# Kernel optimization log

Hardware: AMD Instinct MI355X
Metric: run time of the kernel (lower is better)

## Reference

```python
import jax, jax.numpy as jnp
import numpy as np

B = 8192
NUM_NODES = 100000
EMB = 128
W1D, W2D, W3D = 64, 128, 256   # witness_dims
CODE = 128
HID = 64                        # hardcoded hidden_dim in WitnessExtractor / decoder
TOTW = W1D + W2D + W3D          # 448


def _linear_params(key, fan_in, fan_out):
    k1, k2 = jax.random.split(key)
    bound = 1.0 / np.sqrt(fan_in)
    w = jax.random.uniform(k1, (fan_out, fan_in), jnp.float32, -bound, bound)
    b = jax.random.uniform(k2, (fan_out,), jnp.float32, -bound, bound)
    return w, b


def setup_inputs() -> dict:
    key = jax.random.key(0)
    ks = jax.random.split(key, 12)
    u = jax.random.randint(ks[0], (B,), 0, NUM_NODES, dtype=jnp.int64 if jax.config.jax_enable_x64 else jnp.int32)
    v = jax.random.randint(ks[1], (B,), 0, NUM_NODES, dtype=u.dtype)
    emb = jax.random.normal(ks[2], (NUM_NODES, EMB), jnp.float32)
    e1_w1, e1_b1 = _linear_params(ks[3], 2 * EMB, HID)
    e1_w2, e1_b2 = _linear_params(ks[4], HID, W1D)
    e2_w1, e2_b1 = _linear_params(ks[5], 2 * EMB + W1D, HID)
    e2_w2, e2_b2 = _linear_params(ks[6], HID, W2D)
    e3_w1, e3_b1 = _linear_params(ks[7], 2 * EMB + W2D, HID)
    e3_w2, e3_b2 = _linear_params(ks[8], HID, W3D)
    trop_w = jax.random.normal(ks[9], (CODE, TOTW), jnp.float32)  # init_scale=1.0
    dec_w1, dec_b1 = _linear_params(ks[10], CODE, HID)
    dec_w2, dec_b2 = _linear_params(ks[11], HID, 1)
    return dict(u=u, v=v, emb=emb,
                e1_w1=e1_w1, e1_b1=e1_b1, e1_w2=e1_w2, e1_b2=e1_b2,
                e2_w1=e2_w1, e2_b1=e2_b1, e2_w2=e2_w2, e2_b2=e2_b2,
                e3_w1=e3_w1, e3_b1=e3_b1, e3_w2=e3_w2, e3_b2=e3_b2,
                trop_w=trop_w, dec_w1=dec_w1, dec_b1=dec_b1,
                dec_w2=dec_w2, dec_b2=dec_b2)


def _witness(x, w1, b1, w2, b2):
    h = jax.nn.relu(x @ w1.T + b1)
    return jax.nn.sigmoid(h @ w2.T + b2)


def reference(u, v, emb,
              e1_w1, e1_b1, e1_w2, e1_b2,
              e2_w1, e2_b1, e2_w2, e2_b2,
              e3_w1, e3_b1, e3_w2, e3_b2,
              trop_w, dec_w1, dec_b1, dec_w2, dec_b2):
    u_emb = emb[u]                               # [B, EMB]
    v_emb = emb[v]
    base = jnp.concatenate([u_emb, v_emb], axis=1)  # [B, 2*EMB]
    w1 = _witness(base, e1_w1, e1_b1, e1_w2, e1_b2)
    w2 = _witness(jnp.concatenate([base, w1], axis=1), e2_w1, e2_b1, e2_w2, e2_b2)
    w3 = _witness(jnp.concatenate([base, w2], axis=1), e3_w1, e3_b1, e3_w2, e3_b2)
    wit = jnp.concatenate([w1, w2, w3], axis=1)  # [B, TOTW]
    # tropical (min-plus) matmul: code[b,o] = min_j (wit[b,j] + trop_w[o,j])
    code = jnp.min(wit[:, None, :] + trop_w[None, :, :], axis=2)  # [B, CODE]
    h = jax.nn.relu(code @ dec_w1.T + dec_b1)
    return h @ dec_w2.T + dec_b2                 # [B, 1]
```

## Files before the change

### kernel.cpp

```cpp
#include <hip/hip_runtime.h>
#include <hip/hip_fp16.h>
#include <math.h>

#define BATCH 8192
#define EMB 128
#define TILE 16
#define NTHREADS 1024
#define NWAVES 16
#define CH 136
#define WITS 450
#define SLOT 32

#define OFF_E1W1 0
#define OFF_E1W2 16384
#define OFF_E2W1 20480
#define OFF_E2W2 40960
#define OFF_E3W1 49152
#define OFF_E3W2 73728
#define OFF_DW1  90112
#define OFF_DW2  98304
#define W_DENSE  98368

typedef __attribute__((ext_vector_type(8))) _Float16 v8h;
typedef __attribute__((ext_vector_type(4))) float v4f;

struct Smem {
    _Float16 XB[32 * CH];
    _Float16 W12C[24 * CH];
    _Float16 H[8 * CH];
    _Float16 CODE[16 * CH];
    _Float16 WITrm[TILE * WITS];
    unsigned int ent[128 * SLOT];
    unsigned int cnt[128];
};

__global__ __launch_bounds__(1024) void prep_kernel(
    const float* __restrict__ s0, const float* __restrict__ s1,
    const float* __restrict__ s2, const float* __restrict__ s3,
    const float* __restrict__ s4, const float* __restrict__ s5,
    const float* __restrict__ s6, const float* __restrict__ s7,
    const float* __restrict__ trop, _Float16* __restrict__ ws)
{
    const int b = blockIdx.x;
    const int tid = threadIdx.x;
    if (b < 25) {
        const int idx4 = (b * 1024 + tid) * 4;
        if (idx4 >= W_DENSE) return;
        const float* src; int off;
        if      (idx4 < OFF_E1W2) { src = s0; off = OFF_E1W1; }
        else if (idx4 < OFF_E2W1) { src = s1; off = OFF_E1W2; }
        else if (idx4 < OFF_E2W2) { src = s2; off = OFF_E2W1; }
        else if (idx4 < OFF_E3W1) { src = s3; off = OFF_E2W2; }
        else if (idx4 < OFF_E3W2) { src = s4; off = OFF_E3W1; }
        else if (idx4 < OFF_DW1)  { src = s5; off = OFF_E3W2; }
        else if (idx4 < OFF_DW2)  { src = s6; off = OFF_DW1;  }
        else                      { src = s7; off = OFF_DW2;  }
        const float4 v = *(const float4*)(src + (idx4 - off));
        _Float16* dst = ws + idx4;
        dst[0] = (_Float16)v.x; dst[1] = (_Float16)v.y;
        dst[2] = (_Float16)v.z; dst[3] = (_Float16)v.w;
    } else {
        const int lane = tid & 63;
        const int wave = tid >> 6;
        const int o = (b - 25) * 16 + wave;
        if (o >= 128) return;
        unsigned int* base = (unsigned int*)(ws + W_DENSE);

        const float* row = trop + (size_t)o * 448;
        float vals[7];
        float mn = 1e30f;
        #pragma unroll
        for (int it = 0; it < 7; ++it) {
            vals[it] = row[lane + it * 64];
            mn = fminf(mn, vals[it]);
        }
        mn = fminf(mn, __shfl_xor(mn, 1, 64));
        mn = fminf(mn, __shfl_xor(mn, 2, 64));
        mn = fminf(mn, __shfl_xor(mn, 4, 64));
        mn = fminf(mn, __shfl_xor(mn, 8, 64));
        mn = fminf(mn, __shfl_xor(mn, 16, 64));
        mn = fminf(mn, __shfl_xor(mn, 32, 64));
        const float thr = mn + 1.02f;

        const unsigned long long ltmask = (1ull << lane) - 1ull;
        unsigned int pos0 = 0;
        #pragma unroll
        for (int it = 0; it < 7; ++it) {
            const bool sel = vals[it] <= thr;
            const unsigned long long m = __ballot(sel);
            if (sel) {
                const unsigned int pos = pos0 + (unsigned)__popcll(m & ltmask);
                if (pos < SLOT) {
                    const unsigned short hb =
                        __builtin_bit_cast(unsigned short, (_Float16)vals[it]);
                    base[o * SLOT + pos] = ((unsigned)(lane + it * 64) << 16) | hb;
                }
            }
            pos0 += (unsigned)__popcll(m);
        }
        if (lane == 0) base[4096 + o] = pos0;
    }
}

template <int K, int STEPS0, int O, int ACT, bool CHUNKW, bool RMW>
__device__ __forceinline__ void dense_mfma(
    const _Float16* __restrict__ Wg, const float* __restrict__ bias,
    const _Float16* A0, const _Float16* A1,
    _Float16* OutC, _Float16* OutRM, int rmbase, int wave, int lane)
{
    constexpr int STEPS = K / 32;
    static_assert(STEPS % 2 == 0, "even steps");
    constexpr int NJOBS = O / 16;
    const int l15 = lane & 15;
    const int quad = lane >> 4;

    for (int nt = wave; nt < NJOBS; nt += NWAVES) {
        v4f c0 = {0.f, 0.f, 0.f, 0.f};
        v4f c1 = {0.f, 0.f, 0.f, 0.f};
        const _Float16* wrow = Wg + (size_t)(nt * 16 + l15) * K + quad * 8;
        #pragma unroll
        for (int s = 0; s < STEPS; s += 2) {
            const int g0 = s * 4 + quad;
            const int g1 = (s + 1) * 4 + quad;
            const _Float16* a0p = (s < STEPS0)
                ? (A0 + g0 * CH + l15 * 8)
                : (A1 + (g0 - STEPS0 * 4) * CH + l15 * 8);
            const _Float16* a1p = ((s + 1) < STEPS0)
                ? (A0 + g1 * CH + l15 * 8)
                : (A1 + (g1 - STEPS0 * 4) * CH + l15 * 8);
            const v8h a0 = *(const v8h*)a0p;
            const v8h b0 = *(const v8h*)(wrow + s * 32);
            const v8h a1 = *(const v8h*)a1p;
            const v8h b1 = *(const v8h*)(wrow + (s + 1) * 32);
            c0 = __builtin_amdgcn_mfma_f32_16x16x32_f16(a0, b0, c0, 0, 0, 0);
            c1 = __builtin_amdgcn_mfma_f32_16x16x32_f16(a1, b1, c1, 0, 0, 0);
        }
        const v4f c = c0 + c1;
        const int o = nt * 16 + l15;
        const float bs = bias[o];
        #pragma unroll
        for (int i = 0; i < 4; ++i) {
            float vv = c[i] + bs;
            if (ACT == 0) vv = fmaxf(vv, 0.f);
            else          vv = 1.f / (1.f + __expf(-vv));
            const int m = quad * 4 + i;
            const _Float16 hv = (_Float16)vv;
            if (CHUNKW) OutC[(o >> 3) * CH + m * 8 + (o & 7)] = hv;
            if (RMW)    OutRM[m * WITS + rmbase + o] = hv;
        }
    }
}

__global__ __launch_bounds__(NTHREADS, 8) void tacit_fused_kernel(
    const int* __restrict__ u, const int* __restrict__ v,
    const float* __restrict__ emb,
    const float* __restrict__ e1_b1, const float* __restrict__ e1_b2,
    const float* __restrict__ e2_b1, const float* __restrict__ e2_b2,
    const float* __restrict__ e3_b1, const float* __restrict__ e3_b2,
    const float* __restrict__ dec_b1, const float* __restrict__ dec_b2,
    const float* __restrict__ trop,
    const _Float16* __restrict__ ws,
    float* __restrict__ out)
{
    __shared__ Smem S;
    const int tid = threadIdx.x;
    const int lane = tid & 63;
    const int wave = tid >> 6;
    const int row0 = blockIdx.x * TILE;

    {
        const unsigned int* base = (const unsigned int*)(ws + W_DENSE);
        *(uint4*)&S.ent[tid * 4] = *(const uint4*)(base + tid * 4);
        if (tid < 32) *(uint4*)&S.cnt[tid * 4] = *(const uint4*)(base + 4096 + tid * 4);
    }
    if (tid < 512) {
        const int row = tid & 15;
        const int kq = tid >> 4;
        const int node = (kq < 16) ? u[row0 + row] : v[row0 + row];
        const int col = (kq & 15) * 8;
        const float4 f0 = *(const float4*)(emb + (size_t)node * EMB + col);
        const float4 f1 = *(const float4*)(emb + (size_t)node * EMB + col + 4);
        v8h hv;
        hv[0] = (_Float16)f0.x; hv[1] = (_Float16)f0.y;
        hv[2] = (_Float16)f0.z; hv[3] = (_Float16)f0.w;
        hv[4] = (_Float16)f1.x; hv[5] = (_Float16)f1.y;
        hv[6] = (_Float16)f1.z; hv[7] = (_Float16)f1.w;
        *(v8h*)&S.XB[kq * CH + row * 8] = hv;
    }
    __syncthreads();

    dense_mfma<256, 8, 64, 0, true, false>(ws + OFF_E1W1, e1_b1, S.XB, nullptr,
                                           S.H, nullptr, 0, wave, lane);
    __syncthreads();
    dense_mfma<64, 2, 64, 1, true, true>(ws + OFF_E1W2, e1_b2, S.H, nullptr,
                                         S.W12C, S.WITrm, 0, wave, lane);
    __syncthreads();

    dense_mfma<320, 8, 64, 0, true, false>(ws + OFF_E2W1, e2_b1, S.XB, S.W12C,
                                           S.H, nullptr, 0, wave, lane);
    __syncthreads();
    dense_mfma<64, 2, 128, 1, true, true>(ws + OFF_E2W2, e2_b2, S.H, nullptr,
                                          S.W12C + 8 * CH, S.WITrm, 64, wave, lane);
    __syncthreads();

    dense_mfma<384, 8, 64, 0, true, false>(ws + OFF_E3W1, e3_b1, S.XB, S.W12C + 8 * CH,
                                           S.H, nullptr, 0, wave, lane);
    __syncthreads();
    dense_mfma<64, 2, 256, 1, false, true>(ws + OFF_E3W2, e3_b2, S.H, nullptr,
                                           nullptr, S.WITrm, 192, wave, lane);
    __syncthreads();

    {
        const int r = lane & 15;
        const int cp = lane >> 4;
        const _Float16* wrow = &S.WITrm[r * WITS];
        float acc[8];
        int idx[8], end8[8];
        #pragma unroll
        for (int i = 0; i < 8; ++i) {
            const int o = (wave << 3) + i;
            const int n = (int)S.cnt[o];
            idx[i] = o * SLOT + cp;
            end8[i] = o * SLOT + (n < SLOT ? n : SLOT);
            acc[i] = 1e30f;
        }
        bool any = true;
        while (any) {
            any = false;
            #pragma unroll
            for (int i = 0; i < 8; ++i) {
                if (idx[i] < end8[i]) {
                    const unsigned int cwv = S.ent[idx[i]];
                    const int j = (int)(cwv >> 16);
                    const float tv = (float)__builtin_bit_cast(
                        _Float16, (unsigned short)(cwv & 0xffffu));
                    acc[i] = fminf(acc[i], (float)wrow[j] + tv);
                    idx[i] += 4;
                    any = true;
                }
            }
        }
        #pragma unroll
        for (int i = 0; i < 8; ++i) {
            const int o = (wave << 3) + i;
            if ((int)S.cnt[o] > SLOT) {
                const float* trow = trop + (size_t)o * 448;
                for (int j = cp; j < 448; j += 4)
                    acc[i] = fminf(acc[i], (float)wrow[j] + trow[j]);
            }
        }
        #pragma unroll
        for (int i = 0; i < 8; ++i) {
            float a = acc[i];
            a = fminf(a, __shfl_xor(a, 16, 64));
            a = fminf(a, __shfl_xor(a, 32, 64));
            if (cp == 0) {
                const int o = (wave << 3) + i;
                S.CODE[(o >> 3) * CH + r * 8 + (o & 7)] = (_Float16)a;
            }
        }
    }
    __syncthreads();

    dense_mfma<128, 4, 64, 0, true, false>(ws + OFF_DW1, dec_b1, S.CODE, nullptr,
                                           S.H, nullptr, 0, wave, lane);
    __syncthreads();

    if (tid < 64) {
        const int r = lane & 15;
        const int part = lane >> 4;
        const _Float16* w2 = ws + OFF_DW2;
        float s = 0.f;
        #pragma unroll
        for (int q = 0; q < 2; ++q) {
            const int c = part + q * 4;
            const v8h hr = *(const v8h*)(&S.H[c * CH + r * 8]);
            const v8h wr = *(const v8h*)(w2 + c * 8);
            #pragma unroll
            for (int t = 0; t < 8; ++t) s += (float)hr[t] * (float)wr[t];
        }
        s += __shfl_xor(s, 16, 64);
        s += __shfl_xor(s, 32, 64);
        if (part == 0) out[row0 + r] = s + dec_b2[0];
    }
}

extern "C" void kernel_launch(void* const* d_in, const int* in_sizes, int n_in,
                              void* d_out, int out_size, void* d_ws, size_t ws_size,
                              hipStream_t stream) {
    const int*   u      = (const int*)d_in[0];
    const int*   v      = (const int*)d_in[1];
    const float* emb    = (const float*)d_in[2];
    const float* e1_w1  = (const float*)d_in[3];
    const float* e1_b1  = (const float*)d_in[4];
    const float* e1_w2  = (const float*)d_in[5];
    const float* e1_b2  = (const float*)d_in[6];
    const float* e2_w1  = (const float*)d_in[7];
    const float* e2_b1  = (const float*)d_in[8];
    const float* e2_w2  = (const float*)d_in[9];
    const float* e2_b2  = (const float*)d_in[10];
    const float* e3_w1  = (const float*)d_in[11];
    const float* e3_b1  = (const float*)d_in[12];
    const float* e3_w2  = (const float*)d_in[13];
    const float* e3_b2  = (const float*)d_in[14];
    const float* trop_w = (const float*)d_in[15];
    const float* dec_w1 = (const float*)d_in[16];
    const float* dec_b1 = (const float*)d_in[17];
    const float* dec_w2 = (const float*)d_in[18];
    const float* dec_b2 = (const float*)d_in[19];
    float* out = (float*)d_out;
    _Float16* ws = (_Float16*)d_ws;

    prep_kernel<<<33, 1024, 0, stream>>>(
        e1_w1, e1_w2, e2_w1, e2_w2, e3_w1, e3_w2, dec_w1, dec_w2, trop_w, ws);

    tacit_fused_kernel<<<BATCH / TILE, NTHREADS, 0, stream>>>(
        u, v, emb,
        e1_b1, e1_b2, e2_b1, e2_b2, e3_b1, e3_b2, dec_b1, dec_b2,
        trop_w, ws, out);
}
```

Baseline: 151.2 us.

## Compute base-embedding parts of all three first-layer projections in one stage

The base-input (u,v embedding) part of the first linear layer of each of the three witness extractors is now computed together in a single stage across 12 waves. Partial sums for extractors 2 and 3 are stored as fp32 in new shared buffers. The later stages then only multiply the witness-dependent columns (64 or 128) and add the stored partials. This moves dependent serial work into one wider parallel stage and shortens the critical path, at the cost of extra LDS, which may reduce occupancy.

```diff
diff --git a/kernel.cpp b/kernel.cpp
--- a/kernel.cpp
+++ b/kernel.cpp
@@ -10,6 +10,7 @@
 #define CH 136
 #define WITS 450
 #define SLOT 32
+#define PBS 17
 
 #define OFF_E1W1 0
 #define OFF_E1W2 16384
@@ -30,6 +31,8 @@
     _Float16 H[8 * CH];
     _Float16 CODE[16 * CH];
     _Float16 WITrm[TILE * WITS];
+    float PB0[64 * PBS];
+    float PB1[64 * PBS];
     unsigned int ent[128 * SLOT];
     unsigned int cnt[128];
 };
@@ -151,6 +154,87 @@
     }
 }
 
+__device__ __forceinline__ void stage_base3(
+    const _Float16* __restrict__ ws,
+    const float* __restrict__ b1, const float* __restrict__ b2,
+    const float* __restrict__ b3,
+    const _Float16* XB, _Float16* H, float* PB0, float* PB1,
+    int wave, int lane)
+{
+    if (wave >= 12) return;
+    const int tgt = wave >> 2;
+    const int nt  = wave & 3;
+    const int l15 = lane & 15;
+    const int quad = lane >> 4;
+    const int o = nt * 16 + l15;
+    const _Float16* wrow;
+    const float* bias;
+    if (tgt == 0)      { wrow = ws + OFF_E1W1 + (size_t)o * 256; bias = b1; }
+    else if (tgt == 1) { wrow = ws + OFF_E2W1 + (size_t)o * 320; bias = b2; }
+    else               { wrow = ws + OFF_E3W1 + (size_t)o * 384; bias = b3; }
+    wrow += quad * 8;
+    v4f c0 = {0.f, 0.f, 0.f, 0.f};
+    v4f c1 = {0.f, 0.f, 0.f, 0.f};
+    #pragma unroll
+    for (int s = 0; s < 8; s += 2) {
+        const v8h a0 = *(const v8h*)(XB + (s * 4 + quad) * CH + l15 * 8);
+        const v8h b0 = *(const v8h*)(wrow + s * 32);
+        const v8h a1 = *(const v8h*)(XB + ((s + 1) * 4 + quad) * CH + l15 * 8);
+        const v8h b1v = *(const v8h*)(wrow + (s + 1) * 32);
+        c0 = __builtin_amdgcn_mfma_f32_16x16x32_f16(a0, b0, c0, 0, 0, 0);
+        c1 = __builtin_amdgcn_mfma_f32_16x16x32_f16(a1, b1v, c1, 0, 0, 0);
+    }
+    const v4f c = c0 + c1;
+    const float bs = bias[o];
+    if (tgt == 0) {
+        #pragma unroll
+        for (int i = 0; i < 4; ++i) {
+            const float vv = fmaxf(c[i] + bs, 0.f);
+            const int m = quad * 4 + i;
+            H[(o >> 3) * CH + m * 8 + (o & 7)] = (_Float16)vv;
+        }
+    } else {
+        float* PB = (tgt == 1) ? PB0 : PB1;
+        #pragma unroll
+        for (int i = 0; i < 4; ++i)
+            PB[o * PBS + quad * 4 + i] = c[i] + bs;
+    }
+}
+
+template <int KW, int RS>
+__device__ __forceinline__ void dense_addpb(
+    const _Float16* __restrict__ Wg,
+    const _Float16* A0, const float* __restrict__ PB,
+    _Float16* OutH, int wave, int lane)
+{
+    constexpr int STEPS = KW / 32;
+    static_assert(STEPS % 2 == 0, "even steps");
+    if (wave >= 4) return;
+    const int l15 = lane & 15;
+    const int quad = lane >> 4;
+    const int o = wave * 16 + l15;
+    const _Float16* wrow = Wg + (size_t)o * RS + quad * 8;
+    v4f c0, c1 = {0.f, 0.f, 0.f, 0.f};
+    #pragma unroll
+    for (int i = 0; i < 4; ++i) c0[i] = PB[o * PBS + quad * 4 + i];
+    #pragma unroll
+    for (int s = 0; s < STEPS; s += 2) {
+        const v8h a0 = *(const v8h*)(A0 + (s * 4 + quad) * CH + l15 * 8);
+        const v8h b0 = *(const v8h*)(wrow + s * 32);
+        const v8h a1 = *(const v8h*)(A0 + ((s + 1) * 4 + quad) * CH + l15 * 8);
+        const v8h b1 = *(const v8h*)(wrow + (s + 1) * 32);
+        c0 = __builtin_amdgcn_mfma_f32_16x16x32_f16(a0, b0, c0, 0, 0, 0);
+        c1 = __builtin_amdgcn_mfma_f32_16x16x32_f16(a1, b1, c1, 0, 0, 0);
+    }
+    const v4f c = c0 + c1;
+    #pragma unroll
+    for (int i = 0; i < 4; ++i) {
+        const float vv = fmaxf(c[i], 0.f);
+        const int m = quad * 4 + i;
+        OutH[(o >> 3) * CH + m * 8 + (o & 7)] = (_Float16)vv;
+    }
+}
+
 __global__ __launch_bounds__(NTHREADS, 8) void tacit_fused_kernel(
     const int* __restrict__ u, const int* __restrict__ v,
     const float* __restrict__ emb,
@@ -189,23 +273,23 @@
     }
     __syncthreads();
 
-    dense_mfma<256, 8, 64, 0, true, false>(ws + OFF_E1W1, e1_b1, S.XB, nullptr,
-                                           S.H, nullptr, 0, wave, lane);
-    __syncthreads();
+    stage_base3(ws, e1_b1, e2_b1, e3_b1, S.XB, S.H, S.PB0, S.PB1, wave, lane);
+    __syncthreads();
+
     dense_mfma<64, 2, 64, 1, true, true>(ws + OFF_E1W2, e1_b2, S.H, nullptr,
                                          S.W12C, S.WITrm, 0, wave, lane);
     __syncthreads();
 
-    dense_mfma<320, 8, 64, 0, true, false>(ws + OFF_E2W1, e2_b1, S.XB, S.W12C,
-                                           S.H, nullptr, 0, wave, lane);
-    __syncthreads();
+    dense_addpb<64, 320>(ws + OFF_E2W1 + 256, S.W12C, S.PB0, S.H, wave, lane);
+    __syncthreads();
+
     dense_mfma<64, 2, 128, 1, true, true>(ws + OFF_E2W2, e2_b2, S.H, nullptr,
                                           S.W12C + 8 * CH, S.WITrm, 64, wave, lane);
     __syncthreads();
 
-    dense_mfma<384, 8, 64, 0, true, false>(ws + OFF_E3W1, e3_b1, S.XB, S.W12C + 8 * CH,
-                                           S.H, nullptr, 0, wave, lane);
-    __syncthreads();
+    dense_addpb<128, 384>(ws + OFF_E3W1 + 256, S.W12C + 8 * CH, S.PB1, S.H, wave, lane);
+    __syncthreads();
+
     dense_mfma<64, 2, 256, 1, false, true>(ws + OFF_E3W2, e3_b2, S.H, nullptr,
                                            nullptr, S.WITrm, 192, wave, lane);
     __syncthreads();
```

Measured after the change: 150.7 us. About the same (-0.3%).
